# Performance work log

Measured on AMD Instinct MI355X. Metric: run time of the kernel, lower is better.

The kernel has to match this reference:

```python
import jax, jax.numpy as jnp
import numpy as np

F_DIM = 128; HID = 32; C = 8 * HID; DEPTH = 5; K = 3; HEADS = 8
JK_H = (7 * C) // 2  # 896, PyG JumpingKnowledge('lstm', C, jk_depth=7)
FLEX = 512; CLASSES = 10; GATE_H = 21 * HID
BS = 512; NPG = 23; N_NODES = BS * NPG
EPS = 1e-5


def _bn(x, gamma=None, beta=None):
    # training-mode BatchNorm1d (biased variance), affine optional
    mu = x.mean(0)
    var = x.var(0)
    y = (x - mu) * jax.lax.rsqrt(var + EPS)
    return y * gamma + beta if gamma is not None else y


def _lstm(seq, w_ih, w_hh, b_ih, b_hh):
    # seq: [T, N, C] -> hidden states [T, N, H]; torch gate order i,f,g,o
    n = seq.shape[1]
    hdim = w_hh.shape[1]
    def step(carry, xt):
        h, c = carry
        z = xt @ w_ih.T + h @ w_hh.T + b_ih + b_hh
        i, f, g, o = jnp.split(z, 4, axis=-1)
        c = jax.nn.sigmoid(f) * c + jax.nn.sigmoid(i) * jnp.tanh(g)
        h = jax.nn.sigmoid(o) * jnp.tanh(c)
        return (h, c), h
    init = (jnp.zeros((n, hdim), seq.dtype), jnp.zeros((n, hdim), seq.dtype))
    _, hs = jax.lax.scan(step, init, seq)
    return hs


def _forward(x, conv1_w, conv1_b, bn1_g, bn1_b, ll1_w, ll1_b, tag_w, tag_b,
             gat_w, gat_asrc, gat_adst, gat_b,
             lw_ih_f, lw_hh_f, lb_ih_f, lb_hh_f, lw_ih_b, lw_hh_b, lb_ih_b, lb_hh_b,
             jk_w, jk_b, fff_w1, fff_b1, fff_w2, fff_b2,
             gate_w1, gate_b1, gate_w2, gate_b2,
             conv2_w, conv2_b, bn2_g, bn2_b, fc_w, fc_b,
             edge_index, batch, num_graphs):
    n, f = x.shape
    bs = num_graphs
    # --- temporal preprocessing: PE over node axis (d_model=23), Conv1d, BN ---
    xt = x.reshape(bs, NPG, f).transpose(0, 2, 1)            # [bs, F, 23]
    pos = jnp.arange(f, dtype=x.dtype)[:, None]
    div = jnp.exp(jnp.arange(0, NPG, 2, dtype=x.dtype) * (-np.log(10000.0) / NPG))
    pe = jnp.zeros((f, NPG), x.dtype)
    pe = pe.at[:, 0::2].set(jnp.sin(pos * div))
    pe = pe.at[:, 1::2].set(jnp.cos(pos * div)[:, :(NPG - 1) // 2])
    xt = (xt + pe[None]).transpose(0, 2, 1)                  # [bs, 23, F]
    xt = jax.lax.conv_general_dilated(xt, conv1_w, (1,), [(1, 1)],
            dimension_numbers=('NCH', 'OIH', 'NCH')) + conv1_b[None, :, None]
    h = _bn(xt.reshape(n, f), bn1_g, bn1_b) @ ll1_w + ll1_b  # [N, HID]
    # --- symmetric gcn_norm (no self loops) shared by all TAGConv layers ---
    src, dst = edge_index[0], edge_index[1]
    deg = jax.ops.segment_sum(jnp.ones(src.shape, h.dtype), dst, n)
    dinv = jnp.where(deg > 0, jax.lax.rsqrt(jnp.maximum(deg, 1.0)), 0.0)
    wnorm = dinv[src] * dinv[dst]                            # [E]
    # GAT uses self loops
    loop = jnp.arange(n, dtype=src.dtype)
    src_sl = jnp.concatenate([src, loop])
    dst_sl = jnp.concatenate([dst, loop])

    jk_seq = []
    for i in range(DEPTH):
        # TAGConv: concat powers of normalized adjacency, then linear
        xs = h
        feats = [h]
        for _ in range(K):
            xs = jax.ops.segment_sum(wnorm[:, None] * xs[src], dst, n)
            feats.append(xs)
        tag = jnp.concatenate(feats, axis=-1) @ tag_w[i] + tag_b[i]
        h = _bn(h + tag)                                     # SublayerConnection (BN affine=False)
        # GATConv, heads=8, concat
        g = (h @ gat_w[i]).reshape(n, HEADS, HID)
        a = jax.nn.leaky_relu((g * gat_asrc[i]).sum(-1)[src_sl]
                              + (g * gat_adst[i]).sum(-1)[dst_sl], 0.2)  # [E', heads]
        m = jax.lax.stop_gradient(jax.ops.segment_max(a, dst_sl, n))
        ea = jnp.exp(a - m[dst_sl])
        alpha = ea / jax.ops.segment_sum(ea, dst_sl, n)[dst_sl]
        out = jax.ops.segment_sum(alpha[:, :, None] * g[src_sl], dst_sl, n)
        jk_seq.append(out.reshape(n, C) + gat_b[i])

    # JumpingKnowledge 'lstm': bi-LSTM attention over the DEPTH layer outputs
    seq = jnp.stack(jk_seq, axis=0)                          # [T=5, N, C]
    hf = _lstm(seq, lw_ih_f, lw_hh_f, lb_ih_f, lb_hh_f)
    hb = _lstm(seq[::-1], lw_ih_b, lw_hh_b, lb_ih_b, lb_hh_b)[::-1]
    att = (jnp.concatenate([hf, hb], -1) @ jk_w + jk_b)[..., 0]  # [T, N]
    w_jk = jax.nn.softmax(att, axis=0)                       # softmax over layers
    xg = (seq * w_jk[:, :, None]).sum(0)                     # [N, C]
    # FinalFeedForward + residual BN (slc4)
    ff = jax.nn.elu(xg @ fff_w1 + fff_b1) @ fff_w2 + fff_b2
    xg = _bn(xg + ff)
    # GlobalAttention pooling per graph
    gate = ((xg @ gate_w1 + gate_b1) @ gate_w2 + gate_b2)[:, 0]  # [N]
    gm = jax.lax.stop_gradient(jax.ops.segment_max(gate, batch, bs))
    ge = jnp.exp(gate - gm[batch])
    gw = ge / jax.ops.segment_sum(ge, batch, bs)[batch]
    pooled = jax.ops.segment_sum(gw[:, None] * xg, batch, bs)    # [bs, C]
    # Conv1d(1->10, k=9) over channel axis, mean over out-channels, BN, classifier
    y = jax.lax.conv_general_dilated(pooled[:, None, :], conv2_w, (1,), [(4, 4)],
            dimension_numbers=('NCH', 'OIH', 'NCH')) + conv2_b[None, :, None]
    y = _bn(y.mean(axis=1), bn2_g, bn2_b)
    return jax.nn.log_softmax(y @ fc_w + fc_b, axis=1)


def setup_inputs() -> dict:
    key = jax.random.key(0)
    it = iter(jax.random.split(key, 48))
    def rn(shape, scale=0.05):
        return jax.random.normal(next(it), shape, dtype=jnp.float32) * scale
    # complete digraph (no self loops) inside each 23-node graph
    s, d = np.meshgrid(np.arange(NPG), np.arange(NPG), indexing='ij')
    mask = s != d
    s, d = s[mask], d[mask]
    off = (np.arange(BS) * NPG)[:, None]
    src = (off + s[None, :]).reshape(-1)
    dst = (off + d[None, :]).reshape(-1)
    edge_index = jnp.asarray(np.stack([src, dst]), dtype=jnp.int32)
    batch = jnp.repeat(jnp.arange(BS, dtype=jnp.int32), NPG)
    return dict(
        x=rn((N_NODES, F_DIM), 1.0),
        edge_index=edge_index, batch=batch, num_graphs=BS,
        conv1_w=rn((NPG, NPG, 3)), conv1_b=rn((NPG,)),
        bn1_g=jnp.ones((F_DIM,), jnp.float32), bn1_b=jnp.zeros((F_DIM,), jnp.float32),
        ll1_w=rn((F_DIM, HID)), ll1_b=rn((HID,)),
        tag_w=rn((DEPTH, (K + 1) * HID, HID)), tag_b=rn((DEPTH, HID)),
        gat_w=rn((DEPTH, HID, HEADS * HID)), gat_asrc=rn((DEPTH, HEADS, HID)),
        gat_adst=rn((DEPTH, HEADS, HID)), gat_b=rn((DEPTH, HEADS * HID)),
        lw_ih_f=rn((4 * JK_H, C)), lw_hh_f=rn((4 * JK_H, JK_H)),
        lb_ih_f=rn((4 * JK_H,)), lb_hh_f=rn((4 * JK_H,)),
        lw_ih_b=rn((4 * JK_H, C)), lw_hh_b=rn((4 * JK_H, JK_H)),
        lb_ih_b=rn((4 * JK_H,)), lb_hh_b=rn((4 * JK_H,)),
        jk_w=rn((2 * JK_H, 1)), jk_b=rn((1,)),
        fff_w1=rn((C, FLEX)), fff_b1=rn((FLEX,)),
        fff_w2=rn((FLEX, C)), fff_b2=rn((C,)),
        gate_w1=rn((C, GATE_H)), gate_b1=rn((GATE_H,)),
        gate_w2=rn((GATE_H, 1)), gate_b2=rn((1,)),
        conv2_w=rn((10, 1, 9)), conv2_b=rn((10,)),
        bn2_g=jnp.ones((C,), jnp.float32), bn2_b=jnp.zeros((C,), jnp.float32),
        fc_w=rn((C, CLASSES)), fc_b=rn((CLASSES,)),
    )


def reference(x, edge_index, batch, num_graphs, conv1_w, conv1_b, bn1_g, bn1_b,
              ll1_w, ll1_b, tag_w, tag_b, gat_w, gat_asrc, gat_adst, gat_b,
              lw_ih_f, lw_hh_f, lb_ih_f, lb_hh_f, lw_ih_b, lw_hh_b, lb_ih_b, lb_hh_b,
              jk_w, jk_b, fff_w1, fff_b1, fff_w2, fff_b2,
              gate_w1, gate_b1, gate_w2, gate_b2,
              conv2_w, conv2_b, bn2_g, bn2_b, fc_w, fc_b):
    return _forward(x, conv1_w, conv1_b, bn1_g, bn1_b, ll1_w, ll1_b, tag_w, tag_b,
                    gat_w, gat_asrc, gat_adst, gat_b,
                    lw_ih_f, lw_hh_f, lb_ih_f, lb_hh_f, lw_ih_b, lw_hh_b, lb_ih_b, lb_hh_b,
                    jk_w, jk_b, fff_w1, fff_b1, fff_w2, fff_b2,
                    gate_w1, gate_b1, gate_w2, gate_b2,
                    conv2_w, conv2_b, bn2_g, bn2_b, fc_w, fc_b,
                    edge_index, batch, num_graphs)
```

## Files before the change

kernel.cpp:

```cpp
#include <hip/hip_runtime.h>
#include <math.h>

#define NNODES 11776
#define NGR    512
#define NPG    23
#define FDIM   128
#define HID    32
#define CDIM   256
#define JKH    896
#define ZCOLS  3584
#define EPSBN  1e-5f

typedef long long i64;
typedef unsigned short ushort_t;
typedef __attribute__((ext_vector_type(8))) short bf16x8;
typedef __attribute__((ext_vector_type(4))) float f32x4;

__device__ __forceinline__ float fsig(float x) { return 1.f / (1.f + __expf(-x)); }
__device__ __forceinline__ float ftanh(float x) {
  x = fminf(fmaxf(x, -15.f), 15.f);
  float e = __expf(2.f * x);
  return (e - 1.f) / (e + 1.f);
}

__device__ __forceinline__ ushort_t f2bf(float x) {
  unsigned u = __float_as_uint(x);
  return (ushort_t)((u + 0x7fffu + ((u >> 16) & 1u)) >> 16);
}
__device__ __forceinline__ float bf2f(ushort_t b) {
  return __uint_as_float(((unsigned)b) << 16);
}

__device__ __forceinline__ void gload16(const ushort_t* g, ushort_t* l) {
  __builtin_amdgcn_global_load_lds(
      (const __attribute__((address_space(1))) void*)g,
      (__attribute__((address_space(3))) void*)l, 16, 0, 0);
}

__global__ __launch_bounds__(256) void conv1_kernel(
    const float* __restrict__ x, const float* __restrict__ w,
    const float* __restrict__ bias, float* __restrict__ out,
    float* __restrict__ stats) {
  int b = blockIdx.x;
  __shared__ float in[NPG][FDIM];
  __shared__ float wsh[NPG * NPG * 3];
  __shared__ float cs[FDIM], cq[FDIM];
  int tid = threadIdx.x;
  if (tid < FDIM) { cs[tid] = 0.f; cq[tid] = 0.f; }
  const float c0 = -2.f * logf(10000.f) / 23.f;
  for (int idx = tid; idx < NPG * FDIM; idx += 256) {
    int p = idx >> 7, f = idx & 127;
    int j = p >> 1;
    float ang = (float)f * expf(c0 * (float)j);
    float pe = (p & 1) ? cosf(ang) : sinf(ang);
    in[p][f] = x[(i64)(b * NPG + p) * FDIM + f] + pe;
  }
  for (int idx = tid; idx < NPG * NPG * 3; idx += 256) wsh[idx] = w[idx];
  __syncthreads();
  float ls = 0.f, lq = 0.f;
  int fme = tid & 127;
  for (int idx = tid; idx < NPG * FDIM; idx += 256) {
    int o = idx >> 7, f = idx & 127;
    float acc = bias[o];
    for (int i = 0; i < NPG; ++i) {
      const float* wr = &wsh[(o * NPG + i) * 3];
      float s = in[i][f] * wr[1];
      if (f > 0)   s += in[i][f - 1] * wr[0];
      if (f < 127) s += in[i][f + 1] * wr[2];
      acc += s;
    }
    out[(i64)(b * NPG + o) * FDIM + f] = acc;
    ls += acc; lq += acc * acc;
  }
  atomicAdd(&cs[fme], ls);
  atomicAdd(&cq[fme], lq);
  __syncthreads();
  if (tid < FDIM) {
    atomicAdd(&stats[tid], cs[tid]);
    atomicAdd(&stats[FDIM + tid], cq[tid]);
  }
}

__global__ __launch_bounds__(256) void fold_ll1(
    const float* __restrict__ acc, const float* __restrict__ g,
    const float* __restrict__ be, const float* __restrict__ w,
    const float* __restrict__ lb, float* __restrict__ Wp, float* __restrict__ bp) {
  int tid = threadIdx.x;
  const float invR = 1.f / (float)NNODES;
  for (int idx = tid; idx < FDIM * HID; idx += 256) {
    int k = idx >> 5;
    float mu = acc[k] * invR;
    float var = acc[FDIM + k] * invR - mu * mu;
    float scale = g[k] * rsqrtf(var + EPSBN);
    Wp[idx] = scale * w[idx];
  }
  if (tid < HID) {
    float s = lb[tid];
    for (int k = 0; k < FDIM; ++k) {
      float mu = acc[k] * invR;
      float var = acc[FDIM + k] * invR - mu * mu;
      float scale = g[k] * rsqrtf(var + EPSBN);
      s += (be[k] - mu * scale) * w[k * HID + tid];
    }
    bp[tid] = s;
  }
}

template <int BT>
__global__ __launch_bounds__(256) void sgemm(
    const float* __restrict__ A, const float* __restrict__ B, float* __restrict__ C,
    int M, int N, int K,
    const float* __restrict__ bias, const float* __restrict__ resid,
    int act, int accumulate) {
  __shared__ float As[16][128];
  __shared__ float Bs[16][128];
  int tid = threadIdx.x;
  int bm0 = blockIdx.x * 128;
  int bn0 = blockIdx.y * 128;
  int tx = tid & 15, ty = tid >> 4;
  float acc[8][8];
#pragma unroll
  for (int i = 0; i < 8; ++i)
#pragma unroll
    for (int j = 0; j < 8; ++j) acc[i][j] = 0.f;

  int ar = tid >> 2;
  int akc = (tid & 3) << 2;
  bool bfull = (bn0 + 127 < N);

  for (int k0 = 0; k0 < K; k0 += 16) {
    {
      const float* ap = A + (i64)(bm0 + ar) * K + k0 + akc;
      float4 a0 = *(const float4*)ap;
      float4 a1 = *(const float4*)(ap + (i64)64 * K);
      As[akc + 0][ar] = a0.x; As[akc + 1][ar] = a0.y;
      As[akc + 2][ar] = a0.z; As[akc + 3][ar] = a0.w;
      As[akc + 0][ar + 64] = a1.x; As[akc + 1][ar + 64] = a1.y;
      As[akc + 2][ar + 64] = a1.z; As[akc + 3][ar + 64] = a1.w;
    }
    if (BT) {
      int br = tid >> 1;
      int bkc = (tid & 1) << 3;
      const float* bp = B + (i64)(bn0 + br) * K + k0 + bkc;
      float4 b0 = *(const float4*)bp;
      float4 b1 = *(const float4*)(bp + 4);
      Bs[bkc + 0][br] = b0.x; Bs[bkc + 1][br] = b0.y;
      Bs[bkc + 2][br] = b0.z; Bs[bkc + 3][br] = b0.w;
      Bs[bkc + 4][br] = b1.x; Bs[bkc + 5][br] = b1.y;
      Bs[bkc + 6][br] = b1.z; Bs[bkc + 7][br] = b1.w;
    } else {
      int bk = tid >> 4;
      int bn = (tid & 15) << 3;
      const float* bp = B + (i64)(k0 + bk) * N + bn0 + bn;
      if (bfull) {
        *(float4*)&Bs[bk][bn] = *(const float4*)bp;
        *(float4*)&Bs[bk][bn + 4] = *(const float4*)(bp + 4);
      } else {
#pragma unroll
        for (int q = 0; q < 8; ++q)
          Bs[bk][bn + q] = (bn0 + bn + q < N) ? bp[q] : 0.f;
      }
    }
    __syncthreads();
#pragma unroll
    for (int kk = 0; kk < 16; ++kk) {
      float a[8], b[8];
      *(float4*)(a)     = *(const float4*)&As[kk][ty * 8];
      *(float4*)(a + 4) = *(const float4*)&As[kk][ty * 8 + 4];
      *(float4*)(b)     = *(const float4*)&Bs[kk][tx * 8];
      *(float4*)(b + 4) = *(const float4*)&Bs[kk][tx * 8 + 4];
#pragma unroll
      for (int i = 0; i < 8; ++i)
#pragma unroll
        for (int j = 0; j < 8; ++j)
          acc[i][j] = fmaf(a[i], b[j], acc[i][j]);
    }
    __syncthreads();
  }
#pragma unroll
  for (int i = 0; i < 8; ++i) {
    int m = bm0 + ty * 8 + i;
#pragma unroll
    for (int j = 0; j < 8; ++j) {
      int n = bn0 + tx * 8 + j;
      if (n < N) {
        i64 ci = (i64)m * N + n;
        float v = acc[i][j];
        if (accumulate) {
          C[ci] += v;
        } else {
          if (bias) v += bias[n];
          if (act == 1) v = v > 0.f ? v : expm1f(v);
          if (resid) v += resid[ci];
          C[ci] = v;
        }
      }
    }
  }
}

__global__ __launch_bounds__(256) void tag_fused(
    const float* __restrict__ hbuf, const float* __restrict__ tag_w,
    const float* __restrict__ tag_b, float* __restrict__ hres,
    float* __restrict__ stats) {
  int b = blockIdx.x, tid = threadIdx.x;
  __shared__ float fe[NPG][FDIM];
  __shared__ float wsh[FDIM * HID];
  __shared__ float S[HID];
  __shared__ float cs[HID], cq[HID];
  if (tid < HID) { cs[tid] = 0.f; cq[tid] = 0.f; }
  const float* hp = hbuf + (i64)b * NPG * HID;
  for (int idx = tid; idx < NPG * HID; idx += 256) fe[idx >> 5][idx & 31] = hp[idx];
  for (int idx = tid; idx < FDIM * HID; idx += 256) wsh[idx] = tag_w[idx];
  __syncthreads();
  if (tid < HID) {
    float s = 0.f;
    for (int p = 0; p < NPG; ++p) s += fe[p][tid];
    S[tid] = s;
  }
  __syncthreads();
  const float wn = 1.f / 22.f;
  for (int idx = tid; idx < NPG * HID; idx += 256) {
    int p = idx >> 5, c = idx & 31;
    float f0 = fe[p][c], Sc = S[c];
    float f1 = (Sc - f0) * wn;
    float f2 = (Sc - f1) * wn;
    float f3 = (Sc - f2) * wn;
    fe[p][HID + c] = f1;
    fe[p][2 * HID + c] = f2;
    fe[p][3 * HID + c] = f3;
  }
  __syncthreads();
  for (int idx = tid; idx < NPG * HID; idx += 256) {
    int p = idx >> 5, c = idx & 31;
    float acc = tag_b[c];
#pragma unroll 8
    for (int k = 0; k < FDIM; ++k) acc += fe[p][k] * wsh[k * HID + c];
    float v = fe[p][c] + acc;
    hres[(i64)(b * NPG + p) * HID + c] = v;
    atomicAdd(&cs[c], v);
    atomicAdd(&cq[c], v * v);
  }
  __syncthreads();
  if (tid < HID) {
    atomicAdd(&stats[tid], cs[tid]);
    atomicAdd(&stats[HID + tid], cq[tid]);
  }
}

__global__ __launch_bounds__(256) void gat_tag_fused(
    const float* __restrict__ hres, const float* __restrict__ stats,
    const float* __restrict__ gat_w, const float* __restrict__ asrc,
    const float* __restrict__ adst, const float* __restrict__ gbias,
    ushort_t* __restrict__ outseq,
    const float* __restrict__ tag_w_next, const float* __restrict__ tag_b_next,
    float* __restrict__ hres_out, float* __restrict__ stats_next, int has_next) {
  int b = blockIdx.x, tid = threadIdx.x;
  __shared__ float hn[NPG * HID];
  __shared__ float ssrc[NPG * 8], sdst[NPG * 8], sinv[NPG * 8];
  __shared__ float buf[10120];
  __shared__ float S[HID], cs[HID], cq[HID];
  float* gsh = buf;
  float* ealpha = buf + 5888;
  const float invR = 1.f / (float)NNODES;
  for (int idx = tid; idx < NPG * HID; idx += 256) {
    int c = idx & 31;
    float mu = stats[c] * invR;
    float var = stats[HID + c] * invR - mu * mu;
    hn[idx] = (hres[(i64)b * NPG * HID + idx] - mu) * rsqrtf(var + EPSBN);
  }
  __syncthreads();
  for (int idx = tid; idx < NPG * CDIM; idx += 256) {
    int p = idx >> 8, d = idx & 255;
    float acc = 0.f;
#pragma unroll
    for (int k = 0; k < HID; ++k) acc += hn[p * HID + k] * gat_w[k * CDIM + d];
    gsh[idx] = acc;
  }
  __syncthreads();
  if (tid < NPG * 8) {
    int p = tid >> 3, hd = tid & 7;
    float s1 = 0.f, s2 = 0.f;
    const float* gp = &gsh[p * CDIM + hd * 32];
#pragma unroll
    for (int d = 0; d < 32; ++d) {
      s1 += gp[d] * asrc[hd * 32 + d];
      s2 += gp[d] * adst[hd * 32 + d];
    }
    ssrc[tid] = s1;
    sdst[tid] = s2;
  }
  __syncthreads();
  if (tid < NPG * 8) {
    int v = tid >> 3, hd = tid & 7;
    float sd = sdst[v * 8 + hd];
    float e[NPG];
    float m = -1e30f;
#pragma unroll
    for (int u = 0; u < NPG; ++u) {
      float xv = ssrc[u * 8 + hd] + sd;
      xv = xv > 0.f ? xv : 0.2f * xv;
      e[u] = xv;
      m = fmaxf(m, xv);
    }
    float s = 0.f;
#pragma unroll
    for (int u = 0; u < NPG; ++u) {
      float t = __expf(e[u] - m);
      ealpha[(v * NPG + u) * 8 + hd] = t;
      s += t;
    }
    sinv[tid] = 1.f / s;
  }
  __syncthreads();
  {
    int hd = tid >> 5, d = tid & 31;
    const i64 base = (i64)b * NPG * CDIM;
    for (int v = 0; v < NPG; ++v) {
      float acc = 0.f;
#pragma unroll
      for (int u = 0; u < NPG; ++u)
        acc += ealpha[(v * NPG + u) * 8 + hd] * gsh[u * CDIM + hd * 32 + d];
      outseq[base + (i64)v * CDIM + hd * 32 + d] =
          f2bf(acc * sinv[v * 8 + hd] + gbias[hd * 32 + d]);
    }
  }
  if (!has_next) return;
  __syncthreads();
  float* fe = buf;
  float* wsh = buf + 2944;
  if (tid < HID) { cs[tid] = 0.f; cq[tid] = 0.f; }
  for (int idx = tid; idx < FDIM * HID; idx += 256) wsh[idx] = tag_w_next[idx];
  for (int idx = tid; idx < NPG * HID; idx += 256)
    fe[(idx >> 5) * FDIM + (idx & 31)] = hn[idx];
  __syncthreads();
  if (tid < HID) {
    float s = 0.f;
    for (int p = 0; p < NPG; ++p) s += fe[p * FDIM + tid];
    S[tid] = s;
  }
  __syncthreads();
  const float wn = 1.f / 22.f;
  for (int idx = tid; idx < NPG * HID; idx += 256) {
    int p = idx >> 5, c = idx & 31;
    float f0 = fe[p * FDIM + c], Sc = S[c];
    float f1 = (Sc - f0) * wn;
    float f2 = (Sc - f1) * wn;
    float f3 = (Sc - f2) * wn;
    fe[p * FDIM + HID + c] = f1;
    fe[p * FDIM + 2 * HID + c] = f2;
    fe[p * FDIM + 3 * HID + c] = f3;
  }
  __syncthreads();
  for (int idx = tid; idx < NPG * HID; idx += 256) {
    int p = idx >> 5, c = idx & 31;
    float acc = tag_b_next[c];
#pragma unroll 8
    for (int k = 0; k < FDIM; ++k) acc += fe[p * FDIM + k] * wsh[k * HID + c];
    float v = fe[p * FDIM + c] + acc;
    hres_out[(i64)(b * NPG + p) * HID + c] = v;
    atomicAdd(&cs[c], v);
    atomicAdd(&cq[c], v * v);
  }
  __syncthreads();
  if (tid < HID) {
    atomicAdd(&stats_next[tid], cs[tid]);
    atomicAdd(&stats_next[HID + tid], cq[tid]);
  }
}

__global__ void pack_w(const float* __restrict__ w, ushort_t* __restrict__ wp,
                       int ldK) {
  i64 total = (i64)ZCOLS * ldK;
  i64 idx = (i64)blockIdx.x * 256 + threadIdx.x;
  i64 stride = (i64)gridDim.x * 256;
  for (; idx < total; idx += stride) {
    int r = (int)(idx / ldK), k = (int)(idx % ldK);
    int g = r / JKH, jj = r % JKH;
    int p = (jj >> 4) * 64 + g * 16 + (jj & 15);
    wp[(i64)p * ldK + k] = f2bf(w[idx]);
  }
}

__global__ void pack_t(const float* __restrict__ w, ushort_t* __restrict__ wt,
                       int K, int N) {
  i64 total = (i64)K * N;
  i64 idx = (i64)blockIdx.x * 256 + threadIdx.x;
  i64 stride = (i64)gridDim.x * 256;
  for (; idx < total; idx += stride) {
    int k = (int)(idx / N), n = (int)(idx % N);
    wt[(i64)n * K + k] = f2bf(w[idx]);
  }
}

__global__ __launch_bounds__(256) void small_prep(
    const float* __restrict__ gw1, const float* __restrict__ gb1,
    const float* __restrict__ gw2, const float* __restrict__ gb2,
    float* __restrict__ gatev, float* __restrict__ gateb0,
    const float* __restrict__ cw, const float* __restrict__ cb,
    float* __restrict__ wbar,
    const float* __restrict__ bi0, const float* __restrict__ bh0,
    float* __restrict__ bp0,
    const float* __restrict__ bi1, const float* __restrict__ bh1,
    float* __restrict__ bp1) {
  int blk = blockIdx.x, tid = threadIdx.x;
  if (blk == 0) {
    float s = 0.f;
    for (int j = 0; j < 672; ++j) s += gw1[tid * 672 + j] * gw2[j];
    gatev[tid] = s;
    float p = 0.f;
    for (int j = tid; j < 672; j += 256) p += gb1[j] * gw2[j];
    __shared__ float sh[4];
#pragma unroll
    for (int o = 32; o > 0; o >>= 1) p += __shfl_down(p, o, 64);
    if ((tid & 63) == 0) sh[tid >> 6] = p;
    __syncthreads();
    if (tid == 0) gateb0[0] = sh[0] + sh[1] + sh[2] + sh[3] + gb2[0];
  } else if (blk == 1) {
    if (tid < 9) {
      float s = 0.f;
      for (int o = 0; o < 10; ++o) s += cw[o * 9 + tid];
      wbar[tid] = s * 0.1f;
    } else if (tid == 9) {
      float s = 0.f;
      for (int o = 0; o < 10; ++o) s += cb[o];
      wbar[9] = s * 0.1f;
    }
  } else {
    for (int r = (blk - 2) * 256 + tid; r < 2 * ZCOLS; r += 15 * 256) {
      int d = r / ZCOLS, rr = r % ZCOLS;
      int g = rr / JKH, jj = rr % JKH;
      int p = (jj >> 4) * 64 + g * 16 + (jj & 15);
      if (d == 0) bp0[p] = bi0[rr] + bh0[rr];
      else        bp1[p] = bi1[rr] + bh1[rr];
    }
  }
}

template <int HASH>
__global__ __launch_bounds__(256) void lstm_step(
    const ushort_t* __restrict__ Aseq,
    const ushort_t* __restrict__ Wih,
    const ushort_t* __restrict__ Hprev,
    const ushort_t* __restrict__ Whh,
    const float*  __restrict__ bspk,
    float* __restrict__ Cst,
    ushort_t* __restrict__ Hout,
    const float* __restrict__ jkw,
    float* __restrict__ attp) {
  __shared__ ushort_t As[128 * 64];
  __shared__ ushort_t Bs[128 * 64];
  __shared__ float att_s[128];
  int tid = threadIdx.x;
  int w = tid >> 6, lane = tid & 63;
  int m0 = blockIdx.y * 128;
  int n0 = blockIdx.x * 128;
  f32x4 acc[4][4];
#pragma unroll
  for (int a = 0; a < 4; ++a)
#pragma unroll
    for (int b = 0; b < 4; ++b) acc[a][b] = (f32x4){0.f, 0.f, 0.f, 0.f};

  const ushort_t* aptr = Aseq;
  const ushort_t* bptr = Wih;
  int lda = CDIM, K = CDIM;
  for (int phase = 0; phase < (HASH ? 2 : 1); ++phase) {
    for (int k0 = 0; k0 < K; k0 += 64) {
#pragma unroll
      for (int i = 0; i < 4; ++i) {
        int r = w + i * 4;
        int s = r * 64 + lane;
        int row = s >> 3;
        int kc = (s & 7) ^ (row & 7);
        gload16(aptr + (i64)(m0 + row) * lda + k0 + kc * 8, &As[r * 512]);
        gload16(bptr + (i64)(n0 + row) * lda + k0 + kc * 8, &Bs[r * 512]);
      }
      __syncthreads();
#pragma unroll
      for (int ks = 0; ks < 2; ++ks) {
        bf16x8 af[4], bfr[4];
        int kq = ks * 4 + (lane >> 4);
#pragma unroll
        for (int mi = 0; mi < 4; ++mi) {
          int row = (w & 1) * 64 + mi * 16 + (lane & 15);
          int pos = row * 8 + (kq ^ (row & 7));
          af[mi] = *(const bf16x8*)&As[pos * 8];
        }
#pragma unroll
        for (int ni = 0; ni < 4; ++ni) {
          int row = (w >> 1) * 64 + ni * 16 + (lane & 15);
          int pos = row * 8 + (kq ^ (row & 7));
          bfr[ni] = *(const bf16x8*)&Bs[pos * 8];
        }
#pragma unroll
        for (int mi = 0; mi < 4; ++mi)
#pragma unroll
          for (int ni = 0; ni < 4; ++ni)
            acc[mi][ni] = __builtin_amdgcn_mfma_f32_16x16x32_bf16(
                af[mi], bfr[ni], acc[mi][ni], 0, 0, 0);
      }
      __syncthreads();
    }
    aptr = Hprev; bptr = Whh; lda = JKH; K = JKH;
  }

  if (tid < 128) att_s[tid] = 0.f;
  __syncthreads();

  int jb = (n0 >> 6) + (w >> 1);
  int j = jb * 16 + (lane & 15);
  float jw = jkw[j];
  float bsi = bspk[jb * 64 + (lane & 15)];
  float bsf = bspk[jb * 64 + 16 + (lane & 15)];
  float bsg = bspk[jb * 64 + 32 + (lane & 15)];
  float bso = bspk[jb * 64 + 48 + (lane & 15)];
#pragma unroll
  for (int mi = 0; mi < 4; ++mi) {
#pragma unroll
    for (int reg = 0; reg < 4; ++reg) {
      int mloc = (w & 1) * 64 + mi * 16 + (lane >> 4) * 4 + reg;
      int m = m0 + mloc;
      float zi = acc[mi][0][reg] + bsi;
      float zf = acc[mi][1][reg] + bsf;
      float zg = acc[mi][2][reg] + bsg;
      float zo = acc[mi][3][reg] + bso;
      i64 ci = (i64)m * JKH + j;
      float cv = fsig(zi) * ftanh(zg);
      if (HASH) cv += fsig(zf) * Cst[ci];
      Cst[ci] = cv;
      float hv = fsig(zo) * ftanh(cv);
      Hout[ci] = f2bf(hv);
      float av = hv * jw;
      av += __shfl_xor(av, 1, 64);
      av += __shfl_xor(av, 2, 64);
      av += __shfl_xor(av, 4, 64);
      av += __shfl_xor(av, 8, 64);
      if ((lane & 15) == 0) atomicAdd(&att_s[mloc], av);
    }
  }
  __syncthreads();
  if (tid < 128) atomicAdd(&attp[m0 + tid], att_s[tid]);
}

template <int ACT, int BF16OUT, int STATS>
__global__ __launch_bounds__(256) void mfma_gemm(
    const ushort_t* __restrict__ A, const ushort_t* __restrict__ Bt, int K,
    const float* __restrict__ bias, const float* __restrict__ resid,
    float* __restrict__ Cf, ushort_t* __restrict__ Cb, int N,
    float* __restrict__ stats) {
  __shared__ ushort_t As[128 * 64];
  __shared__ ushort_t Bs[128 * 64];
  __shared__ float cs[128], cq[128];
  int tid = threadIdx.x;
  int w = tid >> 6, lane = tid & 63;
  int m0 = blockIdx.y * 128;
  int n0 = blockIdx.x * 128;
  f32x4 acc[4][4];
#pragma unroll
  for (int a = 0; a < 4; ++a)
#pragma unroll
    for (int b = 0; b < 4; ++b) acc[a][b] = (f32x4){0.f, 0.f, 0.f, 0.f};

  for (int k0 = 0; k0 < K; k0 += 64) {
#pragma unroll
    for (int i = 0; i < 4; ++i) {
      int r = w + i * 4;
      int s = r * 64 + lane;
      int row = s >> 3;
      int kc = (s & 7) ^ (row & 7);
      gload16(A + (i64)(m0 + row) * K + k0 + kc * 8, &As[r * 512]);
      gload16(Bt + (i64)(n0 + row) * K + k0 + kc * 8, &Bs[r * 512]);
    }
    __syncthreads();
#pragma unroll
    for (int ks = 0; ks < 2; ++ks) {
      bf16x8 af[4], bfr[4];
      int kq = ks * 4 + (lane >> 4);
#pragma unroll
      for (int mi = 0; mi < 4; ++mi) {
        int row = (w & 1) * 64 + mi * 16 + (lane & 15);
        int pos = row * 8 + (kq ^ (row & 7));
        af[mi] = *(const bf16x8*)&As[pos * 8];
      }
#pragma unroll
      for (int ni = 0; ni < 4; ++ni) {
        int row = (w >> 1) * 64 + ni * 16 + (lane & 15);
        int pos = row * 8 + (kq ^ (row & 7));
        bfr[ni] = *(const bf16x8*)&Bs[pos * 8];
      }
#pragma unroll
      for (int mi = 0; mi < 4; ++mi)
#pragma unroll
        for (int ni = 0; ni < 4; ++ni)
          acc[mi][ni] = __builtin_amdgcn_mfma_f32_16x16x32_bf16(
              af[mi], bfr[ni], acc[mi][ni], 0, 0, 0);
    }
    __syncthreads();
  }
  if (STATS) {
    if (tid < 128) { cs[tid] = 0.f; cq[tid] = 0.f; }
    __syncthreads();
  }
#pragma unroll
  for (int ni = 0; ni < 4; ++ni) {
    int nloc = (w >> 1) * 64 + ni * 16 + (lane & 15);
    int n = n0 + nloc;
    float bv = bias[n];
    float s = 0.f, q = 0.f;
#pragma unroll
    for (int mi = 0; mi < 4; ++mi) {
#pragma unroll
      for (int reg = 0; reg < 4; ++reg) {
        int m = m0 + (w & 1) * 64 + mi * 16 + (lane >> 4) * 4 + reg;
        float v = acc[mi][ni][reg] + bv;
        if (ACT) v = v > 0.f ? v : expm1f(v);
        i64 ci = (i64)m * N + n;
        if (BF16OUT) Cb[ci] = f2bf(v);
        else {
          v += resid[ci];
          Cf[ci] = v;
          if (STATS) { s += v; q += v * v; }
        }
      }
    }
    if (STATS) { atomicAdd(&cs[nloc], s); atomicAdd(&cq[nloc], q); }
  }
  if (STATS) {
    __syncthreads();
    if (tid < 128) {
      atomicAdd(&stats[n0 + tid], cs[tid]);
      atomicAdd(&stats[N + n0 + tid], cq[tid]);
    }
  }
}

__global__ __launch_bounds__(256) void jk_combine(const float* __restrict__ att,
                                                  const ushort_t* __restrict__ seq,
                                                  float* __restrict__ xg,
                                                  ushort_t* __restrict__ xgb) {
  int n = blockIdx.x, c = threadIdx.x;
  float a[5];
  float m = -1e30f;
#pragma unroll
  for (int t = 0; t < 5; ++t) {
    a[t] = att[(i64)t * NNODES + n] + att[(i64)(5 + t) * NNODES + n];
    m = fmaxf(m, a[t]);
  }
  float s = 0.f;
#pragma unroll
  for (int t = 0; t < 5; ++t) { a[t] = __expf(a[t] - m); s += a[t]; }
  float inv = 1.f / s;
  float acc = 0.f;
#pragma unroll
  for (int t = 0; t < 5; ++t)
    acc += bf2f(seq[((i64)t * NNODES + n) * CDIM + c]) * (a[t] * inv);
  xg[(i64)n * CDIM + c] = acc;
  xgb[(i64)n * CDIM + c] = f2bf(acc);
}

__global__ void fill0(float* __restrict__ p, i64 nfloat) {
  i64 i = (i64)blockIdx.x * 256 + threadIdx.x;
  i64 stride = (i64)gridDim.x * 256;
  for (; i < nfloat; i += stride) p[i] = 0.f;
}

__global__ __launch_bounds__(256) void pool_kernel(
    const float* __restrict__ s4, const float* __restrict__ st,
    const float* __restrict__ v, const float* __restrict__ b0,
    float* __restrict__ pooled) {
  int g = blockIdx.x, tid = threadIdx.x;
  __shared__ float xn[NPG][CDIM];
  __shared__ float gw[NPG];
  __shared__ float sh[4];
  const float invR = 1.f / (float)NNODES;
  float mu = st[tid] * invR;
  float var = st[CDIM + tid] * invR - mu * mu;
  float rs = rsqrtf(var + EPSBN);
  for (int p = 0; p < NPG; ++p)
    xn[p][tid] = (s4[(i64)(g * NPG + p) * CDIM + tid] - mu) * rs;
  __syncthreads();
  float myv = v[tid];
  for (int p = 0; p < NPG; ++p) {
    float val = xn[p][tid] * myv;
#pragma unroll
    for (int o = 32; o > 0; o >>= 1) val += __shfl_down(val, o, 64);
    if ((tid & 63) == 0) sh[tid >> 6] = val;
    __syncthreads();
    if (tid == 0) gw[p] = sh[0] + sh[1] + sh[2] + sh[3] + b0[0];
    __syncthreads();
  }
  if (tid == 0) {
    float m = -1e30f;
    for (int p = 0; p < NPG; ++p) m = fmaxf(m, gw[p]);
    float s = 0.f;
    for (int p = 0; p < NPG; ++p) { gw[p] = __expf(gw[p] - m); s += gw[p]; }
    float inv = 1.f / s;
    for (int p = 0; p < NPG; ++p) gw[p] *= inv;
  }
  __syncthreads();
  float acc = 0.f;
  for (int p = 0; p < NPG; ++p) acc += gw[p] * xn[p][tid];
  pooled[(i64)g * CDIM + tid] = acc;
}

__global__ __launch_bounds__(256) void conv2mean(const float* __restrict__ pooled,
                                                 const float* __restrict__ wbar,
                                                 float* __restrict__ y2,
                                                 float* __restrict__ st5) {
  int b = blockIdx.x, h = threadIdx.x;
  __shared__ float row[CDIM];
  row[h] = pooled[(i64)b * CDIM + h];
  __syncthreads();
  float s = wbar[9];
#pragma unroll
  for (int t = 0; t < 9; ++t) {
    int hh = h + t - 4;
    if (hh >= 0 && hh < CDIM) s += row[hh] * wbar[t];
  }
  y2[(i64)b * CDIM + h] = s;
  atomicAdd(&st5[h], s);
  atomicAdd(&st5[CDIM + h], s * s);
}

__global__ __launch_bounds__(256) void final_fc(
    const float* __restrict__ y2, const float* __restrict__ acc,
    const float* __restrict__ g2, const float* __restrict__ b2,
    const float* __restrict__ fcw, const float* __restrict__ fcb,
    float* __restrict__ out) {
  int b = blockIdx.x, tid = threadIdx.x;
  __shared__ float yn[CDIM];
  __shared__ float logits[10];
  __shared__ float red[2];
  float mu = acc[tid] / 512.f;
  float var = acc[CDIM + tid] / 512.f - mu * mu;
  yn[tid] = (y2[(i64)b * CDIM + tid] - mu) * rsqrtf(var + EPSBN) * g2[tid] + b2[tid];
  __syncthreads();
  if (tid < 10) {
    float s = fcb[tid];
    for (int h = 0; h < CDIM; ++h) s += yn[h] * fcw[h * 10 + tid];
    logits[tid] = s;
  }
  __syncthreads();
  if (tid == 0) {
    float m = -1e30f;
    for (int o = 0; o < 10; ++o) m = fmaxf(m, logits[o]);
    float s = 0.f;
    for (int o = 0; o < 10; ++o) s += expf(logits[o] - m);
    red[0] = m;
    red[1] = logf(s);
  }
  __syncthreads();
  if (tid < 10) out[(i64)b * 10 + tid] = logits[tid] - red[0] - red[1];
}

extern "C" void kernel_launch(void* const* d_in, const int* in_sizes, int n_in,
                              void* d_out, int out_size, void* d_ws, size_t ws_size,
                              hipStream_t stream) {
  (void)in_sizes; (void)n_in; (void)out_size;
  const float* x        = (const float*)d_in[0];
  const float* conv1_w  = (const float*)d_in[4];
  const float* conv1_b  = (const float*)d_in[5];
  const float* bn1_g    = (const float*)d_in[6];
  const float* bn1_b    = (const float*)d_in[7];
  const float* ll1_w    = (const float*)d_in[8];
  const float* ll1_b    = (const float*)d_in[9];
  const float* tag_w    = (const float*)d_in[10];
  const float* tag_b    = (const float*)d_in[11];
  const float* gat_w    = (const float*)d_in[12];
  const float* gat_asrc = (const float*)d_in[13];
  const float* gat_adst = (const float*)d_in[14];
  const float* gat_b    = (const float*)d_in[15];
  const float* lw_ih[2] = {(const float*)d_in[16], (const float*)d_in[20]};
  const float* lw_hh[2] = {(const float*)d_in[17], (const float*)d_in[21]};
  const float* lb_ih[2] = {(const float*)d_in[18], (const float*)d_in[22]};
  const float* lb_hh[2] = {(const float*)d_in[19], (const float*)d_in[23]};
  const float* jk_w     = (const float*)d_in[24];
  const float* fff_w1   = (const float*)d_in[26];
  const float* fff_b1   = (const float*)d_in[27];
  const float* fff_w2   = (const float*)d_in[28];
  const float* fff_b2   = (const float*)d_in[29];
  const float* gate_w1  = (const float*)d_in[30];
  const float* gate_b1  = (const float*)d_in[31];
  const float* gate_w2  = (const float*)d_in[32];
  const float* gate_b2  = (const float*)d_in[33];
  const float* conv2_w  = (const float*)d_in[34];
  const float* conv2_b  = (const float*)d_in[35];
  const float* bn2_g    = (const float*)d_in[36];
  const float* bn2_b    = (const float*)d_in[37];
  const float* fc_w     = (const float*)d_in[38];
  const float* fc_b     = (const float*)d_in[39];
  float* out = (float*)d_out;

  float* ws = (float*)d_ws;
  i64 off = 0;
  auto alloc = [&](i64 n) { float* p = ws + off; off += (n + 15) & ~(i64)15; return p; };
  ushort_t* seqb = (ushort_t*)alloc(7536640);
  float* att = alloc(10 * NNODES);
  float* st1 = alloc(256);
  float* st2 = alloc(6 * 64);
  float* st4 = alloc(512);
  float* st5 = alloc(512);
  i64 zcount = (i64)(st5 - att) + 512;
  float* xg     = alloc((i64)NNODES * CDIM);
  ushort_t* xgb = (ushort_t*)alloc((i64)NNODES * CDIM / 2);
  float* hbuf   = alloc((i64)NNODES * HID);
  float* hres   = alloc((i64)NNODES * HID);
  float* Wp     = alloc(FDIM * HID);
  float* bp     = alloc(64);
  ushort_t* wihb[2]; ushort_t* whhb[2]; float* bspk[2];
  for (int d = 0; d < 2; ++d) {
    wihb[d] = (ushort_t*)alloc((i64)ZCOLS * CDIM / 2);
    whhb[d] = (ushort_t*)alloc((i64)ZCOLS * JKH / 2);
    bspk[d] = alloc(ZCOLS);
  }
  ushort_t* w1t = (ushort_t*)alloc(512 * 256 / 2);
  ushort_t* w2t = (ushort_t*)alloc(256 * 512 / 2);
  float* gatev  = alloc(CDIM);
  float* gateb0 = alloc(16);
  float* wbar   = alloc(16);
  float* pooled = alloc((i64)NGR * CDIM);
  float* y2     = alloc((i64)NGR * CDIM);
  float* Zs = ws + off;
  i64 S = (i64)(ws_size / 4) - off;
  if (S < 0) S = 0;

  int Tch = (int)(S / 229376); if (Tch < 1) Tch = 1; if (Tch > 92) Tch = 92;
  i64 Sff = S - 3014656;
  int Tf = (int)(Sff / 32768); if (Tf < 1) Tf = 1; if (Tf > 92) Tf = 92;

  float* xconv = Zs;
  ushort_t* hA = (ushort_t*)Zs;
  ushort_t* hB = hA + (i64)Tch * 128 * JKH;
  float* cch   = (float*)(hB + (i64)Tch * 128 * JKH);
  float* s4  = Zs;
  ushort_t* ff1b = (ushort_t*)(s4 + 3014656);

  fill0<<<512, 256, 0, stream>>>(att, zcount);
  for (int d = 0; d < 2; ++d) {
    pack_w<<<2048, 256, 0, stream>>>(lw_ih[d], wihb[d], CDIM);
    pack_w<<<4096, 256, 0, stream>>>(lw_hh[d], whhb[d], JKH);
  }
  pack_t<<<512, 256, 0, stream>>>(fff_w1, w1t, CDIM, 512);
  pack_t<<<512, 256, 0, stream>>>(fff_w2, w2t, 512, CDIM);
  small_prep<<<17, 256, 0, stream>>>(gate_w1, gate_b1, gate_w2, gate_b2,
                                     gatev, gateb0, conv2_w, conv2_b, wbar,
                                     lb_ih[0], lb_hh[0], bspk[0],
                                     lb_ih[1], lb_hh[1], bspk[1]);

  conv1_kernel<<<NGR, 256, 0, stream>>>(x, conv1_w, conv1_b, xconv, st1);
  fold_ll1<<<1, 256, 0, stream>>>(st1, bn1_g, bn1_b, ll1_w, ll1_b, Wp, bp);
  sgemm<0><<<dim3(92, 1), 256, 0, stream>>>(xconv, Wp, hbuf, NNODES, HID, FDIM,
                                            bp, nullptr, 0, 0);

  tag_fused<<<NGR, 256, 0, stream>>>(hbuf, tag_w, tag_b, hres, st2);
  for (int i = 0; i < 5; ++i) {
    int nx = (i < 4) ? (i + 1) : 0;
    gat_tag_fused<<<NGR, 256, 0, stream>>>(
        hres, st2 + i * 64, gat_w + (i64)i * HID * CDIM,
        gat_asrc + i * 256, gat_adst + i * 256, gat_b + i * 256,
        seqb + (i64)i * NNODES * CDIM,
        tag_w + (i64)nx * FDIM * HID, tag_b + nx * HID,
        hres, st2 + (i + 1) * 64, (i < 4) ? 1 : 0);
  }

  for (int dir = 0; dir < 2; ++dir) {
    for (int t0 = 0; t0 < 92; t0 += Tch) {
      int tiles = (92 - t0 < Tch) ? (92 - t0) : Tch;
      i64 r0 = (i64)t0 * 128;
      ushort_t* hp[2] = {hA, hB};
      for (int t = 0; t < 5; ++t) {
        int ts = dir ? 4 - t : t;
        const ushort_t* Ax = seqb + ((i64)ts * NNODES + r0) * CDIM;
        float* attp = att + (i64)(dir * 5 + ts) * NNODES + r0;
        if (t == 0)
          lstm_step<0><<<dim3(28, tiles), 256, 0, stream>>>(
              Ax, wihb[dir], nullptr, nullptr, bspk[dir], cch, hp[0],
              jk_w + dir * JKH, attp);
        else
          lstm_step<1><<<dim3(28, tiles), 256, 0, stream>>>(
              Ax, wihb[dir], hp[(t + 1) & 1], whhb[dir], bspk[dir], cch, hp[t & 1],
              jk_w + dir * JKH, attp);
      }
    }
  }
  jk_combine<<<NNODES, 256, 0, stream>>>(att, seqb, xg, xgb);

  for (int t0 = 0; t0 < 92; t0 += Tf) {
    int tiles = (92 - t0 < Tf) ? (92 - t0) : Tf;
    i64 r0 = (i64)t0 * 128;
    mfma_gemm<1, 1, 0><<<dim3(4, tiles), 256, 0, stream>>>(
        xgb + r0 * CDIM, w1t, CDIM, fff_b1, nullptr, nullptr, ff1b, 512, nullptr);
    mfma_gemm<0, 0, 1><<<dim3(2, tiles), 256, 0, stream>>>(
        ff1b, w2t, 512, fff_b2, xg + r0 * CDIM, s4 + r0 * CDIM, nullptr, CDIM, st4);
  }

  pool_kernel<<<NGR, 256, 0, stream>>>(s4, st4, gatev, gateb0, pooled);
  conv2mean<<<NGR, 256, 0, stream>>>(pooled, wbar, y2, st5);
  final_fc<<<NGR, 256, 0, stream>>>(y2, st5, bn2_g, bn2_b, fc_w, fc_b, out);
}
```

Measured before the change: 1.697 ms.

## Switch LSTM step GEMM to 32x32x16 MFMA with regrouped gate packing

The LSTM step kernel moves from 16x16x32 bf16 MFMA tiles to 32x32x16 tiles, so each wave owns 32 rows and all 128 columns (four gate groups of 32). Weight and bias packing now interleave gates in groups of 32 columns instead of 16, and the epilogue index mapping and attention reduction change to match. The aim is fewer LDS fragment loads per MFMA and better MFMA throughput. In exchange, each wave now reloads the full B tile from LDS, and the epilogue reduction needs an extra shuffle.

```diff
diff --git a/kernel.cpp b/kernel.cpp
--- a/kernel.cpp
+++ b/kernel.cpp
@@ -15,6 +15,7 @@
 typedef unsigned short ushort_t;
 typedef __attribute__((ext_vector_type(8))) short bf16x8;
 typedef __attribute__((ext_vector_type(4))) float f32x4;
+typedef __attribute__((ext_vector_type(16))) float f32x16;
 
 __device__ __forceinline__ float fsig(float x) { return 1.f / (1.f + __expf(-x)); }
 __device__ __forceinline__ float ftanh(float x) {
@@ -377,7 +378,7 @@
   for (; idx < total; idx += stride) {
     int r = (int)(idx / ldK), k = (int)(idx % ldK);
     int g = r / JKH, jj = r % JKH;
-    int p = (jj >> 4) * 64 + g * 16 + (jj & 15);
+    int p = (jj >> 5) * 128 + g * 32 + (jj & 31);
     wp[(i64)p * ldK + k] = f2bf(w[idx]);
   }
 }
@@ -430,7 +431,7 @@
     for (int r = (blk - 2) * 256 + tid; r < 2 * ZCOLS; r += 15 * 256) {
       int d = r / ZCOLS, rr = r % ZCOLS;
       int g = rr / JKH, jj = rr % JKH;
-      int p = (jj >> 4) * 64 + g * 16 + (jj & 15);
+      int p = (jj >> 5) * 128 + g * 32 + (jj & 31);
       if (d == 0) bp0[p] = bi0[rr] + bh0[rr];
       else        bp1[p] = bi1[rr] + bh1[rr];
     }
@@ -455,11 +456,11 @@
   int w = tid >> 6, lane = tid & 63;
   int m0 = blockIdx.y * 128;
   int n0 = blockIdx.x * 128;
-  f32x4 acc[4][4];
-#pragma unroll
-  for (int a = 0; a < 4; ++a)
-#pragma unroll
-    for (int b = 0; b < 4; ++b) acc[a][b] = (f32x4){0.f, 0.f, 0.f, 0.f};
+  f32x16 acc[4];
+#pragma unroll
+  for (int g = 0; g < 4; ++g)
+#pragma unroll
+    for (int r = 0; r < 16; ++r) acc[g][r] = 0.f;
 
   const ushort_t* aptr = Aseq;
   const ushort_t* bptr = Wih;
@@ -477,27 +478,21 @@
       }
       __syncthreads();
 #pragma unroll
-      for (int ks = 0; ks < 2; ++ks) {
-        bf16x8 af[4], bfr[4];
-        int kq = ks * 4 + (lane >> 4);
-#pragma unroll
-        for (int mi = 0; mi < 4; ++mi) {
-          int row = (w & 1) * 64 + mi * 16 + (lane & 15);
-          int pos = row * 8 + (kq ^ (row & 7));
-          af[mi] = *(const bf16x8*)&As[pos * 8];
+      for (int s = 0; s < 4; ++s) {
+        int o = s * 2 + (lane >> 5);
+        bf16x8 af;
+        {
+          int row = w * 32 + (lane & 31);
+          int pos = row * 8 + (o ^ (row & 7));
+          af = *(const bf16x8*)&As[pos * 8];
         }
 #pragma unroll
-        for (int ni = 0; ni < 4; ++ni) {
-          int row = (w >> 1) * 64 + ni * 16 + (lane & 15);
-          int pos = row * 8 + (kq ^ (row & 7));
-          bfr[ni] = *(const bf16x8*)&Bs[pos * 8];
+        for (int g = 0; g < 4; ++g) {
+          int row = g * 32 + (lane & 31);
+          int pos = row * 8 + (o ^ (row & 7));
+          bf16x8 bfr = *(const bf16x8*)&Bs[pos * 8];
+          acc[g] = __builtin_amdgcn_mfma_f32_32x32x16_bf16(af, bfr, acc[g], 0, 0, 0);
         }
-#pragma unroll
-        for (int mi = 0; mi < 4; ++mi)
-#pragma unroll
-          for (int ni = 0; ni < 4; ++ni)
-            acc[mi][ni] = __builtin_amdgcn_mfma_f32_16x16x32_bf16(
-                af[mi], bfr[ni], acc[mi][ni], 0, 0, 0);
       }
       __syncthreads();
     }
@@ -507,36 +502,34 @@
   if (tid < 128) att_s[tid] = 0.f;
   __syncthreads();
 
-  int jb = (n0 >> 6) + (w >> 1);
-  int j = jb * 16 + (lane & 15);
+  int col = lane & 31;
+  int j = blockIdx.x * 32 + col;
   float jw = jkw[j];
-  float bsi = bspk[jb * 64 + (lane & 15)];
-  float bsf = bspk[jb * 64 + 16 + (lane & 15)];
-  float bsg = bspk[jb * 64 + 32 + (lane & 15)];
-  float bso = bspk[jb * 64 + 48 + (lane & 15)];
-#pragma unroll
-  for (int mi = 0; mi < 4; ++mi) {
-#pragma unroll
-    for (int reg = 0; reg < 4; ++reg) {
-      int mloc = (w & 1) * 64 + mi * 16 + (lane >> 4) * 4 + reg;
-      int m = m0 + mloc;
-      float zi = acc[mi][0][reg] + bsi;
-      float zf = acc[mi][1][reg] + bsf;
-      float zg = acc[mi][2][reg] + bsg;
-      float zo = acc[mi][3][reg] + bso;
-      i64 ci = (i64)m * JKH + j;
-      float cv = fsig(zi) * ftanh(zg);
-      if (HASH) cv += fsig(zf) * Cst[ci];
-      Cst[ci] = cv;
-      float hv = fsig(zo) * ftanh(cv);
-      Hout[ci] = f2bf(hv);
-      float av = hv * jw;
-      av += __shfl_xor(av, 1, 64);
-      av += __shfl_xor(av, 2, 64);
-      av += __shfl_xor(av, 4, 64);
-      av += __shfl_xor(av, 8, 64);
-      if ((lane & 15) == 0) atomicAdd(&att_s[mloc], av);
-    }
+  float bsi = bspk[n0 + col];
+  float bsf = bspk[n0 + 32 + col];
+  float bsg = bspk[n0 + 64 + col];
+  float bso = bspk[n0 + 96 + col];
+#pragma unroll
+  for (int reg = 0; reg < 16; ++reg) {
+    int mloc = w * 32 + (reg & 3) + 8 * (reg >> 2) + 4 * (lane >> 5);
+    int m = m0 + mloc;
+    float zi = acc[0][reg] + bsi;
+    float zf = acc[1][reg] + bsf;
+    float zg = acc[2][reg] + bsg;
+    float zo = acc[3][reg] + bso;
+    i64 ci = (i64)m * JKH + j;
+    float cv = fsig(zi) * ftanh(zg);
+    if (HASH) cv += fsig(zf) * Cst[ci];
+    Cst[ci] = cv;
+    float hv = fsig(zo) * ftanh(cv);
+    Hout[ci] = f2bf(hv);
+    float av = hv * jw;
+    av += __shfl_xor(av, 1, 64);
+    av += __shfl_xor(av, 2, 64);
+    av += __shfl_xor(av, 4, 64);
+    av += __shfl_xor(av, 8, 64);
+    av += __shfl_xor(av, 16, 64);
+    if (col == 0) atomicAdd(&att_s[mloc], av);
   }
   __syncthreads();
   if (tid < 128) atomicAdd(&attp[m0 + tid], att_s[tid]);
```

Measured after the change: 1.782 ms. 5.0% more time.
